# Optimization experiments

Measured on AMD Instinct MI355X. Metric: run time of the kernel, lower is better.

The kernel has to match this reference:

```python
import jax, jax.numpy as jnp
import numpy as np

INPUT_SIZE, HIDDEN_SIZE, OUTPUT_SIZE = 256, 512, 256
BATCH, SEQ_LEN = 64, 1024


def _xavier(key, shape):
    fan_out, fan_in = shape
    limit = float(np.sqrt(6.0 / (fan_in + fan_out)))
    return jax.random.uniform(key, shape, jnp.float32, -limit, limit)


def setup_inputs() -> dict:
    key = jax.random.key(0)
    k_x, k_w1, k_w2 = jax.random.split(key, 3)
    x = jax.random.normal(k_x, (BATCH, SEQ_LEN, INPUT_SIZE), jnp.float32)
    W_ih = _xavier(k_w1, (HIDDEN_SIZE, INPUT_SIZE + HIDDEN_SIZE))  # torch Linear weight [out, in]
    b_ih = jnp.zeros((HIDDEN_SIZE,), jnp.float32)
    W_ho = _xavier(k_w2, (OUTPUT_SIZE, HIDDEN_SIZE))
    b_ho = jnp.zeros((OUTPUT_SIZE,), jnp.float32)
    return {"x": x, "W_ih": W_ih, "b_ih": b_ih, "W_ho": W_ho, "b_ho": b_ho}


def reference(x, W_ih, b_ih, W_ho, b_ho):
    batch, seq_len, input_size = x.shape
    hidden = W_ih.shape[0]
    # Split concat-linear into two matmuls: [x_t, h] @ W^T = x_t @ Wx^T + h @ Wh^T
    Wx = W_ih[:, :input_size]   # [H, I]
    Wh = W_ih[:, input_size:]   # [H, H]
    # Precompute input projections for all timesteps: [S, B, H]
    x_proj = jnp.einsum('bsi,hi->sbh', x, Wx) + b_ih

    def step(h, xp_t):
        h_new = jnp.tanh(xp_t + h @ Wh.T)
        return h_new, h_new

    h0 = jnp.zeros((batch, hidden), x.dtype)
    _, hs = jax.lax.scan(step, h0, x_proj)          # hs: [S, B, H]
    hidden_seq = jnp.transpose(hs, (1, 0, 2))       # [B, S, H]
    final_hidden = hidden_seq[:, -1, :]             # [B, H]
    scores = jnp.einsum('bsh,bh->bs', hidden_seq, final_hidden)
    attn = jax.nn.softmax(scores, axis=1)
    context = jnp.einsum('bs,bsh->bh', attn, hidden_seq)
    return context @ W_ho.T + b_ho
```

## Files before the change

kernel.cpp:

```cpp
#include <hip/hip_runtime.h>
#include <cstdint>
#include <cmath>

#define S_LEN 1024
#define BATCH 64
#define IN_SZ 256
#define HID 512
#define OUT_SZ 256
#define WIH_LD 768
#define BH (BATCH * HID)
#define XP_FLOATS (S_LEN * BH)

#define P_REG 176
#define P_LDS 24
#define P_STR_G 14


typedef _Float16 h2v __attribute__((ext_vector_type(2)));
typedef _Float16 f16x8 __attribute__((ext_vector_type(8)));
typedef float f32x4 __attribute__((ext_vector_type(4)));

__device__ __forceinline__ float dot2p(unsigned int a, unsigned int b, float c) {
#if __has_builtin(__builtin_amdgcn_fdot2)
    return __builtin_amdgcn_fdot2(__builtin_bit_cast(h2v, a),
                                  __builtin_bit_cast(h2v, b), c, false);
#else
    h2v av = __builtin_bit_cast(h2v, a);
    h2v bv = __builtin_bit_cast(h2v, b);
    return c + (float)av.x * (float)bv.x + (float)av.y * (float)bv.y;
#endif
}

__global__ __launch_bounds__(256) void pack_w(const float* __restrict__ W_ih,
                                              unsigned int* __restrict__ wstr,
                                              unsigned int* __restrict__ wregbuf,
                                              unsigned int* __restrict__ wldsbuf) {
    int idx = blockIdx.x * 256 + threadIdx.x;
    int p = idx & 255;
    int j = idx >> 8;
    const float* src = W_ih + (size_t)j * WIH_LD + IN_SZ + 2 * p;
    unsigned short lo = __builtin_bit_cast(unsigned short, (_Float16)src[0]);
    unsigned short hi = __builtin_bit_cast(unsigned short, (_Float16)src[1]);
    unsigned int u = (unsigned int)lo | ((unsigned int)hi << 16);
    if (p < P_REG) {
        wregbuf[p * 512 + j] = u;
    } else if (p < P_REG + P_LDS) {
        wldsbuf[(p - P_REG) * 512 + j] = u;
    } else {
        int q = p - (P_REG + P_LDS);
        wstr[((q >> 2) * 512 + j) * 4 + (q & 3)] = u;
    }
}

__global__ __launch_bounds__(256) void pack_wf16(const float* __restrict__ W_ih,
                                                 uint4* __restrict__ wpk) {
    int idx = blockIdx.x * 256 + threadIdx.x;
    if (idx >= 16384) return;
    int nt   = idx >> 9;
    int ks   = (idx >> 6) & 7;
    int lane = idx & 63;
    int n  = nt * 16 + (lane & 15);
    int kb = ks * 32 + (lane >> 4) * 8;
    const float* src = W_ih + (size_t)n * WIH_LD + kb;
    union { uint4 u; _Float16 h[8]; } v;
#pragma unroll
    for (int i = 0; i < 8; ++i) v.h[i] = (_Float16)src[i];
    wpk[idx] = v.u;
}

#define AH_LD 264
__global__ __launch_bounds__(256) void xproj_mfma(const float* __restrict__ x,
                                                  const uint4* __restrict__ wpk,
                                                  const float* __restrict__ b_ih,
                                                  float* __restrict__ xp) {
    const int s    = blockIdx.x;
    const int half = blockIdx.y;
    const int tid  = threadIdx.x;
    __shared__ __align__(16) _Float16 Ah[32 * AH_LD];
    __shared__ float bsh[HID];
    bsh[tid] = b_ih[tid];
    bsh[tid + 256] = b_ih[tid + 256];
    {
        int r  = tid >> 3;
        int c0 = (tid & 7) * 32;
        const float4* s4 = (const float4*)(x + ((size_t)(half * 32 + r) * S_LEN + s) * IN_SZ + c0);
        _Float16* dst = &Ah[r * AH_LD + c0];
#pragma unroll
        for (int i = 0; i < 8; ++i) {
            float4 v = s4[i];
            dst[4 * i + 0] = (_Float16)v.x;
            dst[4 * i + 1] = (_Float16)v.y;
            dst[4 * i + 2] = (_Float16)v.z;
            dst[4 * i + 3] = (_Float16)v.w;
        }
    }
    __syncthreads();
    const int lane = tid & 63;
    const int w    = tid >> 6;
    const int mt   = w & 1;
    const int ntb  = (w >> 1) * 16;
    f16x8 areg[8];
#pragma unroll
    for (int ks = 0; ks < 8; ++ks)
        areg[ks] = *(const f16x8*)&Ah[(mt * 16 + (lane & 15)) * AH_LD + ks * 32 + (lane >> 4) * 8];
    const int brow  = half * 32 + mt * 16 + (lane >> 4) * 4;
    const int ncol0 = lane & 15;
    for (int nt2 = 0; nt2 < 16; ++nt2) {
        int nt = ntb + nt2;
        const uint4* bp = wpk + (size_t)nt * 8 * 64 + lane;
        f32x4 acc = {0.f, 0.f, 0.f, 0.f};
#pragma unroll
        for (int ks = 0; ks < 8; ++ks) {
            uint4 bu = bp[ks * 64];
            acc = __builtin_amdgcn_mfma_f32_16x16x32_f16(
                areg[ks], __builtin_bit_cast(f16x8, bu), acc, 0, 0, 0);
        }
        int n = nt * 16 + ncol0;
        float bias = bsh[n];
        float* outp = xp + (size_t)s * BH + (size_t)brow * HID + n;
#pragma unroll
        for (int r = 0; r < 4; ++r) outp[(size_t)r * HID] = acc[r] + bias;
    }
}

__global__ __launch_bounds__(512, 2) void rnn_f16(const unsigned int* __restrict__ wregbuf,
                                                  const unsigned int* __restrict__ wldsbuf,
                                                  const uint4* __restrict__ wstr,
                                                  float* __restrict__ xp) {
    const int b = blockIdx.x;
    const int j = threadIdx.x;

    __shared__ unsigned int wlds[P_LDS * 512];
    __shared__ unsigned short h2u[2][512];

    unsigned int wreg[P_REG];
#pragma unroll
    for (int p = 0; p < P_REG; ++p) wreg[p] = wregbuf[p * 512 + j];

    for (int g = j; g < P_LDS * 512; g += 512) wlds[g] = wldsbuf[g];
    h2u[0][j] = 0;
    __syncthreads();

    float* col = xp + (size_t)b * HID + j;
    for (int s = 0; s < S_LEN; ++s) {
        const unsigned int* hq = (const unsigned int*)h2u[s & 1];
        float xpv = col[(size_t)s * BH];

        uint4 sw[P_STR_G];
#pragma unroll
        for (int g = 0; g < P_STR_G; ++g) sw[g] = wstr[(size_t)g * 512 + j];

        float a0 = 0.f, a1 = 0.f, a2 = 0.f, a3 = 0.f;
#pragma unroll
        for (int p = 0; p < P_REG; p += 4) {
            a0 = dot2p(wreg[p + 0], hq[p + 0], a0);
            a1 = dot2p(wreg[p + 1], hq[p + 1], a1);
            a2 = dot2p(wreg[p + 2], hq[p + 2], a2);
            a3 = dot2p(wreg[p + 3], hq[p + 3], a3);
        }
#pragma unroll
        for (int p = 0; p < P_LDS; p += 4) {
            a0 = dot2p(wlds[(p + 0) * 512 + j], hq[P_REG + p + 0], a0);
            a1 = dot2p(wlds[(p + 1) * 512 + j], hq[P_REG + p + 1], a1);
            a2 = dot2p(wlds[(p + 2) * 512 + j], hq[P_REG + p + 2], a2);
            a3 = dot2p(wlds[(p + 3) * 512 + j], hq[P_REG + p + 3], a3);
        }
#pragma unroll
        for (int g = 0; g < P_STR_G; ++g) {
            int pb = P_REG + P_LDS + 4 * g;
            a0 = dot2p(sw[g].x, hq[pb + 0], a0);
            a1 = dot2p(sw[g].y, hq[pb + 1], a1);
            a2 = dot2p(sw[g].z, hq[pb + 2], a2);
            a3 = dot2p(sw[g].w, hq[pb + 3], a3);
        }

        float v = tanhf(((a0 + a1) + (a2 + a3)) + xpv);
        col[(size_t)s * BH] = v;
        h2u[(s + 1) & 1][j] = __builtin_bit_cast(unsigned short, (_Float16)v);
        asm volatile("s_waitcnt lgkmcnt(0)" ::: "memory");
        asm volatile("s_barrier" ::: "memory");
    }
}

__global__ __launch_bounds__(256) void attn_sc(const float* __restrict__ hbuf,
                                               float* __restrict__ sc_g) {
    const int b     = blockIdx.x;
    const int chunk = blockIdx.y;
    const int tid   = threadIdx.x;
    const int lane  = tid & 63;
    const int wv    = tid >> 6;
    __shared__ float fh[HID];
    fh[tid] = hbuf[(size_t)(S_LEN - 1) * BH + (size_t)b * HID + tid];
    fh[tid + 256] = hbuf[(size_t)(S_LEN - 1) * BH + (size_t)b * HID + tid + 256];
    __syncthreads();
    float4 f0 = *(const float4*)&fh[lane * 8];
    float4 f1 = *(const float4*)&fh[lane * 8 + 4];
    for (int i = 0; i < 32; ++i) {
        int s = chunk * 128 + wv * 32 + i;
        const float* hr = hbuf + (size_t)s * BH + (size_t)b * HID + lane * 8;
        float4 a0 = *(const float4*)hr;
        float4 a1 = *(const float4*)(hr + 4);
        float p = a0.x * f0.x + a0.y * f0.y + a0.z * f0.z + a0.w * f0.w +
                  a1.x * f1.x + a1.y * f1.y + a1.z * f1.z + a1.w * f1.w;
#pragma unroll
        for (int off = 32; off; off >>= 1) p += __shfl_down(p, off, 64);
        if (lane == 0) sc_g[(size_t)b * S_LEN + s] = p;
    }
}

__global__ __launch_bounds__(256) void attn_ctx(const float* __restrict__ hbuf,
                                                const float* __restrict__ sc_g,
                                                float* __restrict__ ctx_g) {
    const int b   = blockIdx.x;
    const int hc  = blockIdx.y * 128;
    const int tid = threadIdx.x;
    const int lane = tid & 63;
    const int wv   = tid >> 6;
    __shared__ float sc[S_LEN];
    __shared__ float red[4];
    __shared__ float part[256];
    for (int i = tid; i < S_LEN; i += 256) sc[i] = sc_g[(size_t)b * S_LEN + i];
    __syncthreads();
    float m = -1e30f;
    for (int i = tid; i < S_LEN; i += 256) m = fmaxf(m, sc[i]);
#pragma unroll
    for (int off = 32; off; off >>= 1) m = fmaxf(m, __shfl_down(m, off, 64));
    if (lane == 0) red[wv] = m;
    __syncthreads();
    m = fmaxf(fmaxf(red[0], red[1]), fmaxf(red[2], red[3]));
    float sum = 0.f;
    for (int i = tid; i < S_LEN; i += 256) {
        float e = __expf(sc[i] - m);
        sc[i] = e;
        sum += e;
    }
#pragma unroll
    for (int off = 32; off; off >>= 1) sum += __shfl_down(sum, off, 64);
    __syncthreads();
    if (lane == 0) red[wv] = sum;
    __syncthreads();
    float inv = 1.f / (red[0] + red[1] + red[2] + red[3]);
    const int h  = hc + (tid & 127);
    const int sh = tid >> 7;
    const float* hp = hbuf + (size_t)sh * 512 * BH + (size_t)b * HID + h;
    float c = 0.f;
#pragma unroll 4
    for (int s2 = 0; s2 < 512; ++s2)
        c += sc[sh * 512 + s2] * hp[(size_t)s2 * BH];
    part[tid] = c;
    __syncthreads();
    if (tid < 128) ctx_g[(size_t)b * HID + hc + tid] = (part[tid] + part[tid + 128]) * inv;
}

__global__ __launch_bounds__(256) void attn_fin(const float* __restrict__ ctx_g,
                                                const float* __restrict__ W_ho,
                                                const float* __restrict__ b_ho,
                                                float* __restrict__ out) {
    const int b   = blockIdx.x;
    const int tid = threadIdx.x;
    __shared__ float ctx[HID];
    ctx[tid] = ctx_g[(size_t)b * HID + tid];
    ctx[tid + 256] = ctx_g[(size_t)b * HID + tid + 256];
    __syncthreads();
    float o = b_ho[tid];
    const float* wr = W_ho + (size_t)tid * HID;
#pragma unroll 4
    for (int k = 0; k < HID; ++k) o += wr[k] * ctx[k];
    out[(size_t)b * OUT_SZ + tid] = o;
}

extern "C" void kernel_launch(void* const* d_in, const int* in_sizes, int n_in,
                              void* d_out, int out_size, void* d_ws, size_t ws_size,
                              hipStream_t stream) {
    const float* x    = (const float*)d_in[0];
    const float* W_ih = (const float*)d_in[1];
    const float* b_ih = (const float*)d_in[2];
    const float* W_ho = (const float*)d_in[3];
    const float* b_ho = (const float*)d_in[4];
    float* out = (float*)d_out;
    float* ws  = (float*)d_ws;

    float* xp = ws;
    unsigned int* wbase   = (unsigned int*)(ws + XP_FLOATS);
    unsigned int* wstr    = wbase;
    unsigned int* wregbuf = wbase + 28672;
    unsigned int* wldsbuf = wbase + 28672 + P_REG * 512;
    uint4*        wpk     = (uint4*)(wbase + 131072);
    float*        sc_g    = (float*)wbase;
    float*        ctx_g   = (float*)(wbase + 65536);

    pack_w<<<dim3(512), dim3(256), 0, stream>>>(W_ih, wstr, wregbuf, wldsbuf);
    pack_wf16<<<dim3(64), dim3(256), 0, stream>>>(W_ih, wpk);
    xproj_mfma<<<dim3(1024, 2), dim3(256), 0, stream>>>(x, wpk, b_ih, xp);
    rnn_f16<<<dim3(64), dim3(512), 0, stream>>>(wregbuf, wldsbuf, (const uint4*)wstr, xp);
    attn_sc<<<dim3(64, 8), dim3(256), 0, stream>>>(xp, sc_g);
    attn_ctx<<<dim3(64, 4), dim3(256), 0, stream>>>(xp, sc_g, ctx_g);
    attn_fin<<<dim3(64), dim3(256), 0, stream>>>(ctx_g, W_ho, b_ho, out);
}
```

Before: 1.835 ms.

## Drop LDS weight tier, split streamed weights into two overlapped batches, use fast tanh

Removes the LDS-resident slice of the recurrent weights and moves those columns into registers (184) and the global-streamed set (18 groups). The streamed loads are issued in two batches of 9, each interleaved with half of the register dot-products, so load latency can hide behind compute while fewer streamed values are live at once. tanhf is replaced by an exp+reciprocal formula. The gains rely on more registers and better latency hiding; the cost is extra register pressure (risk of spills) and slightly lower tanh accuracy.

```diff
diff --git a/kernel.cpp b/kernel.cpp
--- a/kernel.cpp
+++ b/kernel.cpp
@@ -11,9 +11,9 @@
 #define BH (BATCH * HID)
 #define XP_FLOATS (S_LEN * BH)
 
-#define P_REG 176
-#define P_LDS 24
-#define P_STR_G 14
+#define P_REG 184
+#define P_STR_G 18
+#define P_STR_B 9
 
 
 typedef _Float16 h2v __attribute__((ext_vector_type(2)));
@@ -31,10 +31,19 @@
 #endif
 }
 
+__device__ __forceinline__ float fast_tanh(float x) {
+    float e = __expf(2.0f * x);
+#if __has_builtin(__builtin_amdgcn_rcpf)
+    float r = __builtin_amdgcn_rcpf(e + 1.0f);
+#else
+    float r = 1.0f / (e + 1.0f);
+#endif
+    return __builtin_fmaf(-2.0f, r, 1.0f);
+}
+
 __global__ __launch_bounds__(256) void pack_w(const float* __restrict__ W_ih,
                                               unsigned int* __restrict__ wstr,
-                                              unsigned int* __restrict__ wregbuf,
-                                              unsigned int* __restrict__ wldsbuf) {
+                                              unsigned int* __restrict__ wregbuf) {
     int idx = blockIdx.x * 256 + threadIdx.x;
     int p = idx & 255;
     int j = idx >> 8;
@@ -44,10 +53,8 @@
     unsigned int u = (unsigned int)lo | ((unsigned int)hi << 16);
     if (p < P_REG) {
         wregbuf[p * 512 + j] = u;
-    } else if (p < P_REG + P_LDS) {
-        wldsbuf[(p - P_REG) * 512 + j] = u;
     } else {
-        int q = p - (P_REG + P_LDS);
+        int q = p - P_REG;
         wstr[((q >> 2) * 512 + j) * 4 + (q & 3)] = u;
     }
 }
@@ -124,20 +131,17 @@
 }
 
 __global__ __launch_bounds__(512, 2) void rnn_f16(const unsigned int* __restrict__ wregbuf,
-                                                  const unsigned int* __restrict__ wldsbuf,
                                                   const uint4* __restrict__ wstr,
                                                   float* __restrict__ xp) {
     const int b = blockIdx.x;
     const int j = threadIdx.x;
 
-    __shared__ unsigned int wlds[P_LDS * 512];
     __shared__ unsigned short h2u[2][512];
 
     unsigned int wreg[P_REG];
 #pragma unroll
     for (int p = 0; p < P_REG; ++p) wreg[p] = wregbuf[p * 512 + j];
 
-    for (int g = j; g < P_LDS * 512; g += 512) wlds[g] = wldsbuf[g];
     h2u[0][j] = 0;
     __syncthreads();
 
@@ -146,35 +150,45 @@
         const unsigned int* hq = (const unsigned int*)h2u[s & 1];
         float xpv = col[(size_t)s * BH];
 
-        uint4 sw[P_STR_G];
-#pragma unroll
-        for (int g = 0; g < P_STR_G; ++g) sw[g] = wstr[(size_t)g * 512 + j];
+        uint4 sw[P_STR_B];
+#pragma unroll
+        for (int g = 0; g < P_STR_B; ++g) sw[g] = wstr[(size_t)g * 512 + j];
 
         float a0 = 0.f, a1 = 0.f, a2 = 0.f, a3 = 0.f;
 #pragma unroll
-        for (int p = 0; p < P_REG; p += 4) {
+        for (int p = 0; p < 96; p += 4) {
             a0 = dot2p(wreg[p + 0], hq[p + 0], a0);
             a1 = dot2p(wreg[p + 1], hq[p + 1], a1);
             a2 = dot2p(wreg[p + 2], hq[p + 2], a2);
             a3 = dot2p(wreg[p + 3], hq[p + 3], a3);
         }
 #pragma unroll
-        for (int p = 0; p < P_LDS; p += 4) {
-            a0 = dot2p(wlds[(p + 0) * 512 + j], hq[P_REG + p + 0], a0);
-            a1 = dot2p(wlds[(p + 1) * 512 + j], hq[P_REG + p + 1], a1);
-            a2 = dot2p(wlds[(p + 2) * 512 + j], hq[P_REG + p + 2], a2);
-            a3 = dot2p(wlds[(p + 3) * 512 + j], hq[P_REG + p + 3], a3);
-        }
-#pragma unroll
-        for (int g = 0; g < P_STR_G; ++g) {
-            int pb = P_REG + P_LDS + 4 * g;
+        for (int g = 0; g < P_STR_B; ++g) {
+            int pb = P_REG + 4 * g;
             a0 = dot2p(sw[g].x, hq[pb + 0], a0);
             a1 = dot2p(sw[g].y, hq[pb + 1], a1);
             a2 = dot2p(sw[g].z, hq[pb + 2], a2);
             a3 = dot2p(sw[g].w, hq[pb + 3], a3);
         }
-
-        float v = tanhf(((a0 + a1) + (a2 + a3)) + xpv);
+#pragma unroll
+        for (int g = 0; g < P_STR_B; ++g) sw[g] = wstr[(size_t)(P_STR_B + g) * 512 + j];
+#pragma unroll
+        for (int p = 96; p < P_REG; p += 4) {
+            a0 = dot2p(wreg[p + 0], hq[p + 0], a0);
+            a1 = dot2p(wreg[p + 1], hq[p + 1], a1);
+            a2 = dot2p(wreg[p + 2], hq[p + 2], a2);
+            a3 = dot2p(wreg[p + 3], hq[p + 3], a3);
+        }
+#pragma unroll
+        for (int g = 0; g < P_STR_B; ++g) {
+            int pb = P_REG + 4 * P_STR_B + 4 * g;
+            a0 = dot2p(sw[g].x, hq[pb + 0], a0);
+            a1 = dot2p(sw[g].y, hq[pb + 1], a1);
+            a2 = dot2p(sw[g].z, hq[pb + 2], a2);
+            a3 = dot2p(sw[g].w, hq[pb + 3], a3);
+        }
+
+        float v = fast_tanh(((a0 + a1) + (a2 + a3)) + xpv);
         col[(size_t)s * BH] = v;
         h2u[(s + 1) & 1][j] = __builtin_bit_cast(unsigned short, (_Float16)v);
         asm volatile("s_waitcnt lgkmcnt(0)" ::: "memory");
@@ -283,16 +297,15 @@
     float* xp = ws;
     unsigned int* wbase   = (unsigned int*)(ws + XP_FLOATS);
     unsigned int* wstr    = wbase;
-    unsigned int* wregbuf = wbase + 28672;
-    unsigned int* wldsbuf = wbase + 28672 + P_REG * 512;
+    unsigned int* wregbuf = wbase + P_STR_G * 512 * 4;
     uint4*        wpk     = (uint4*)(wbase + 131072);
     float*        sc_g    = (float*)wbase;
     float*        ctx_g   = (float*)(wbase + 65536);
 
-    pack_w<<<dim3(512), dim3(256), 0, stream>>>(W_ih, wstr, wregbuf, wldsbuf);
+    pack_w<<<dim3(512), dim3(256), 0, stream>>>(W_ih, wstr, wregbuf);
     pack_wf16<<<dim3(64), dim3(256), 0, stream>>>(W_ih, wpk);
     xproj_mfma<<<dim3(1024, 2), dim3(256), 0, stream>>>(x, wpk, b_ih, xp);
-    rnn_f16<<<dim3(64), dim3(512), 0, stream>>>(wregbuf, wldsbuf, (const uint4*)wstr, xp);
+    rnn_f16<<<dim3(64), dim3(512), 0, stream>>>(wregbuf, (const uint4*)wstr, xp);
     attn_sc<<<dim3(64, 8), dim3(256), 0, stream>>>(xp, sc_g);
     attn_ctx<<<dim3(64, 4), dim3(256), 0, stream>>>(xp, sc_g, ctx_g);
     attn_fin<<<dim3(64), dim3(256), 0, stream>>>(ctx_g, W_ho, b_ho, out);
```

New measurement: 3.628 ms. 97.7% more time.
